# Optimization experiments

Measured on AMD Instinct MI355X. Metric: run time of the kernel, lower is better.

Reference implementation:

```python
import jax, jax.numpy as jnp
import numpy as np
from jax import lax

VOCAB, D, H, S, W, OUT = 100000, 300, 50, 64, 32, 5


def setup_inputs() -> dict:
    key = jax.random.key(0)
    ks = jax.random.split(key, 32)
    g = lambda i, shape, scale=0.05: (jax.random.normal(ks[i], shape, dtype=jnp.float32) * scale)
    inp = {
        'doc': jax.random.randint(ks[0], (S, W), 0, VOCAB),
        'emb': g(1, (VOCAB, D)),
        'wl_w': g(2, (H, D)), 'wl_b': g(3, (H,)),
        'c1_w': g(4, (H, H, 1)), 'c1_b': g(5, (H,)),
        'c2_w': g(6, (H, H, 2)), 'c2_b': g(7, (H,)),
        'c3_w': g(8, (H, H, 3)), 'c3_b': g(9, (H,)),
        'f_i_w': g(10, (H, 2 * H)), 'f_i_b': g(11, (H,)),
        'f_f_w': g(12, (H, 2 * H)), 'f_f_b': g(13, (H,)),
        'f_g_w': g(14, (H, 2 * H)), 'f_g_b': g(15, (H,)),
        'b_i_w': g(16, (H, 2 * H)), 'b_i_b': g(17, (H,)),
        'b_f_w': g(18, (H, 2 * H)), 'b_f_b': g(19, (H,)),
        'b_g_w': g(20, (H, 2 * H)), 'b_g_b': g(21, (H,)),
        'out_w': g(22, (OUT, 2 * H)), 'out_b': g(23, (OUT,)),
    }
    return inp


def _conv_rep(x, w, b):
    # x: [S, H, W]; w: [O, I, k] torch-style conv1d weight
    y = lax.conv_general_dilated(x, w, window_strides=(1,), padding='VALID',
                                 dimension_numbers=('NCH', 'OIH', 'NCH'))
    y = y + b[None, :, None]
    return jnp.tanh(y.mean(axis=2))  # [S, H]  (avg-pool over full length then tanh)


def _gnn_scan(reps, Wi, bi, Wf, bf, Wg, bg):
    # reps: [S, H]; sequential gated cell
    def step(h, r):
        comp = jnp.concatenate([r, h])  # [2H]
        i = jax.nn.sigmoid(comp @ Wi.T + bi)
        f = jax.nn.sigmoid(comp @ Wf.T + bf)
        g = jnp.tanh(comp @ Wg.T + bg)
        h_t = jnp.tanh(i * g + f * h)
        return h_t, h_t
    _, hs = lax.scan(step, jnp.zeros(reps.shape[1], dtype=reps.dtype), reps)
    return hs  # [S, H]


def reference(doc, emb, wl_w, wl_b, c1_w, c1_b, c2_w, c2_b, c3_w, c3_b,
              f_i_w, f_i_b, f_f_w, f_f_b, f_g_w, f_g_b,
              b_i_w, b_i_b, b_f_w, b_f_b, b_g_w, b_g_b, out_w, out_b):
    x = emb[doc]                                  # [S, W, D]
    p = jnp.einsum('swd,hd->swh', x, wl_w) + wl_b # word_linear, [S, W, H]
    xc = p.transpose(0, 2, 1)                     # [S, H, W]
    # sentence_convolution: mean over the 3 kernel-size branches
    rep = (_conv_rep(xc, c1_w, c1_b) + _conv_rep(xc, c2_w, c2_b) + _conv_rep(xc, c3_w, c3_b)) / 3.0
    h_f = _gnn_scan(rep, f_i_w, f_i_b, f_f_w, f_f_b, f_g_w, f_g_b)         # forward pass
    h_b = _gnn_scan(rep[::-1], b_i_w, b_i_b, b_f_w, b_f_b, b_g_w, b_g_b)[::-1]  # backward pass, realigned
    gnn_out = jnp.concatenate([h_f, h_b], axis=1).mean(axis=0)             # [2H]
    logits = gnn_out @ out_w.T + out_b
    return jax.nn.softmax(logits)
```

## Files before the change

### kernel.cpp

```cpp
#include <hip/hip_runtime.h>


__device__ __forceinline__ float rl(float v, int j) {
    return __uint_as_float((unsigned)__builtin_amdgcn_readlane(__float_as_uint(v), j));
}
__device__ __forceinline__ float sigm(float x) { return 1.f / (1.f + __expf(-x)); }
__device__ __forceinline__ float tanh_fast(float x) {
    return 1.f - 2.f / (__expf(2.f * x) + 1.f);
}

__global__ __launch_bounds__(320, 1) void rep_kernel(
    const int* __restrict__ doc, const float* __restrict__ emb,
    const float* __restrict__ wl_w, const float* __restrict__ wl_b,
    const float* __restrict__ c1w, const float* __restrict__ c1b,
    const float* __restrict__ c2w, const float* __restrict__ c2b,
    const float* __restrict__ c3w, const float* __restrict__ c3b,
    const float* __restrict__ fiw, const float* __restrict__ fib,
    const float* __restrict__ ffw, const float* __restrict__ ffb,
    const float* __restrict__ fgw, const float* __restrict__ fgb,
    const float* __restrict__ biw, const float* __restrict__ bib,
    const float* __restrict__ bfw, const float* __restrict__ bfb,
    const float* __restrict__ bgw, const float* __restrict__ bgb,
    float* __restrict__ preW)
{
    __shared__ int docs[32];
    __shared__ float xL[32][300];
    __shared__ float sv[5][300];
    __shared__ float P[5][50];
    __shared__ float m[6][50];
    __shared__ float r[50];

    const int s = blockIdx.x, tid = threadIdx.x;
    if (tid < 32) docs[tid] = doc[s * 32 + tid];
    __syncthreads();

    {
        const int w = tid / 10, part = tid - w * 10;
        const float2* row = (const float2*)(emb + docs[w] * 300);
#pragma unroll
        for (int t = 0; t < 15; ++t) {
            float2 v = row[part * 15 + t];
            const int d = (part * 15 + t) * 2;
            xL[w][d]     = v.x;
            xL[w][d + 1] = v.y;
        }
    }
    __syncthreads();

    if (tid < 300) {
        float a = 0.f;
#pragma unroll
        for (int w = 0; w < 32; ++w) a += xL[w][tid];
        sv[0][tid] = a;
        sv[1][tid] = xL[0][tid];
        sv[2][tid] = xL[1][tid];
        sv[3][tid] = xL[30][tid];
        sv[4][tid] = xL[31][tid];
    }
    __syncthreads();

    if (tid < 250) {
        const int i = tid / 5, v = tid - (tid / 5) * 5;
        const float2* wrow = (const float2*)(wl_w + i * 300);
        float a0 = 0.f, a1 = 0.f;
#pragma unroll 5
        for (int d2 = 0; d2 < 150; ++d2) {
            float2 wv = wrow[d2];
            a0 = fmaf(wv.x, sv[v][2 * d2],     a0);
            a1 = fmaf(wv.y, sv[v][2 * d2 + 1], a1);
        }
        P[v][i] = a0 + a1;
    }
    __syncthreads();

    if (tid < 50) {
        const int i = tid;
        const float b  = wl_b[i];
        const float QA = P[0][i], Q0 = P[1][i], Q1 = P[2][i],
                    Q30 = P[3][i], Q31 = P[4][i];
        m[0][i] = QA * (1.f / 32.f) + b;
        m[1][i] = (QA - Q31) * (1.f / 31.f) + b;
        m[2][i] = (QA - Q0)  * (1.f / 31.f) + b;
        m[3][i] = (QA - Q30 - Q31) * (1.f / 30.f) + b;
        m[4][i] = (QA - Q0  - Q31) * (1.f / 30.f) + b;
        m[5][i] = (QA - Q0  - Q1 ) * (1.f / 30.f) + b;
    }
    __syncthreads();

    if (tid < 50) {
        const int o = tid;
        float y1 = c1b[o], y2 = c2b[o], y3 = c3b[o];
        for (int i = 0; i < 50; ++i) {
            y1 = fmaf(c1w[o * 50 + i], m[0][i], y1);
            const float2 w2 = ((const float2*)c2w)[o * 50 + i];
            y2 = fmaf(w2.x, m[1][i], fmaf(w2.y, m[2][i], y2));
            y3 = fmaf(c3w[(o * 50 + i) * 3 + 0], m[3][i], y3);
            y3 = fmaf(c3w[(o * 50 + i) * 3 + 1], m[4][i], y3);
            y3 = fmaf(c3w[(o * 50 + i) * 3 + 2], m[5][i], y3);
        }
        r[o] = (tanh_fast(y1) + tanh_fast(y2) + tanh_fast(y3)) * (1.f / 3.f);
    }
    __syncthreads();

    if (tid < 300) {
        const int g = tid / 50, o = tid - g * 50;
        const float* Wg = (g == 0) ? fiw : (g == 1) ? ffw : (g == 2) ? fgw
                        : (g == 3) ? biw : (g == 4) ? bfw : bgw;
        const float* Bg = (g == 0) ? fib : (g == 1) ? ffb : (g == 2) ? fgb
                        : (g == 3) ? bib : (g == 4) ? bfb : bgb;
        const int sp = (g < 3) ? s : (63 - s);
        const float2* wrow = (const float2*)(Wg + o * 100);
        float acc = Bg[o];
#pragma unroll
        for (int j2 = 0; j2 < 25; ++j2) {
            float2 wv = wrow[j2];
            acc = fmaf(wv.x, r[2 * j2], fmaf(wv.y, r[2 * j2 + 1], acc));
        }
        preW[g * 3200 + sp * 50 + o] = acc;
    }
}

__global__ __launch_bounds__(384, 1) void scan_kernel(
    const float* __restrict__ preW,
    const float* __restrict__ fiw, const float* __restrict__ ffw,
    const float* __restrict__ fgw, const float* __restrict__ biw,
    const float* __restrict__ bfw, const float* __restrict__ bgw,
    const float* __restrict__ out_w, const float* __restrict__ out_b,
    float* __restrict__ outp)
{
    __shared__ float pre[6][64][50];
    __shared__ float aL[2][6][52];
    __shared__ float mh[2][52];
    __shared__ float lg[5];

    const int tid = threadIdx.x;
    const int wv = tid >> 6, lane = tid & 63;
    const int oc = (lane < 50) ? lane : 0;
    const int d  = (wv >= 3) ? 1 : 0;

    {
        const float2* src = (const float2*)preW;
        float2* dst = (float2*)&pre[0][0][0];
#pragma unroll
        for (int k = 0; k < 25; ++k) dst[tid + 384 * k] = src[tid + 384 * k];
    }

    const float* Wg = (wv == 0) ? fiw : (wv == 1) ? ffw : (wv == 2) ? fgw
                    : (wv == 3) ? biw : (wv == 4) ? bfw : bgw;
    float w[50];
    {
        const float2* wrow = (const float2*)(Wg + oc * 100 + 50);
#pragma unroll
        for (int j2 = 0; j2 < 25; ++j2) {
            float2 t = wrow[j2];
            w[2 * j2] = t.x; w[2 * j2 + 1] = t.y;
        }
    }
    __syncthreads();

    float h = 0.f, hsum = 0.f;
    float na = pre[wv][0][oc];
#pragma unroll 1
    for (int s2 = 0; s2 < 64; ++s2) {
        float a0 = na, a1 = 0.f, a2 = 0.f, a3 = 0.f;
        if (s2 < 63) na = pre[wv][s2 + 1][oc];
#pragma unroll
        for (int j = 0; j < 48; j += 4) {
            a0 = fmaf(w[j    ], rl(h, j    ), a0);
            a1 = fmaf(w[j + 1], rl(h, j + 1), a1);
            a2 = fmaf(w[j + 2], rl(h, j + 2), a2);
            a3 = fmaf(w[j + 3], rl(h, j + 3), a3);
        }
        a0 = fmaf(w[48], rl(h, 48), a0);
        a1 = fmaf(w[49], rl(h, 49), a1);
        const float a = (a0 + a1) + (a2 + a3);

        if (lane < 50) aL[s2 & 1][wv][lane] = a;
        __syncthreads();
        const float ai = aL[s2 & 1][d * 3 + 0][oc];
        const float af = aL[s2 & 1][d * 3 + 1][oc];
        const float ag = aL[s2 & 1][d * 3 + 2][oc];
        h = tanh_fast(fmaf(sigm(ai), tanh_fast(ag), sigm(af) * h));
        hsum += h;
    }
    if ((wv == 0 || wv == 3) && lane < 50) mh[d][lane] = hsum * (1.f / 64.f);
    __syncthreads();

    if (tid < 5) {
        const float2* wrow = (const float2*)(out_w + tid * 100);
        float acc = out_b[tid];
#pragma unroll
        for (int j2 = 0; j2 < 25; ++j2) {
            float2 wv2 = wrow[j2];
            acc = fmaf(wv2.x, mh[0][2 * j2], fmaf(wv2.y, mh[0][2 * j2 + 1], acc));
        }
#pragma unroll
        for (int j2 = 0; j2 < 25; ++j2) {
            float2 wv2 = wrow[25 + j2];
            acc = fmaf(wv2.x, mh[1][2 * j2], fmaf(wv2.y, mh[1][2 * j2 + 1], acc));
        }
        lg[tid] = acc;
    }
    __syncthreads();
    if (tid == 0) {
        float mx = lg[0];
#pragma unroll
        for (int k = 1; k < 5; ++k) mx = fmaxf(mx, lg[k]);
        float e[5], se = 0.f;
#pragma unroll
        for (int k = 0; k < 5; ++k) { e[k] = __expf(lg[k] - mx); se += e[k]; }
        const float inv = 1.f / se;
#pragma unroll
        for (int k = 0; k < 5; ++k) outp[k] = e[k] * inv;
    }
}

extern "C" void kernel_launch(void* const* d_in, const int* in_sizes, int n_in,
                              void* d_out, int out_size, void* d_ws, size_t ws_size,
                              hipStream_t stream)
{
    (void)in_sizes; (void)n_in; (void)out_size; (void)ws_size;
    const int*   doc  = (const int*)  d_in[0];
    const float* emb  = (const float*)d_in[1];
    const float* wl_w = (const float*)d_in[2];
    const float* wl_b = (const float*)d_in[3];
    const float* c1w  = (const float*)d_in[4];
    const float* c1b  = (const float*)d_in[5];
    const float* c2w  = (const float*)d_in[6];
    const float* c2b  = (const float*)d_in[7];
    const float* c3w  = (const float*)d_in[8];
    const float* c3b  = (const float*)d_in[9];
    const float* fiw  = (const float*)d_in[10];
    const float* fib  = (const float*)d_in[11];
    const float* ffw  = (const float*)d_in[12];
    const float* ffb  = (const float*)d_in[13];
    const float* fgw  = (const float*)d_in[14];
    const float* fgb  = (const float*)d_in[15];
    const float* biw  = (const float*)d_in[16];
    const float* bib  = (const float*)d_in[17];
    const float* bfw  = (const float*)d_in[18];
    const float* bfb  = (const float*)d_in[19];
    const float* bgw  = (const float*)d_in[20];
    const float* bgb  = (const float*)d_in[21];
    const float* ow   = (const float*)d_in[22];
    const float* ob   = (const float*)d_in[23];

    float* preW = (float*)d_ws;

    rep_kernel<<<64, 320, 0, stream>>>(doc, emb, wl_w, wl_b,
                                       c1w, c1b, c2w, c2b, c3w, c3b,
                                       fiw, fib, ffw, ffb, fgw, fgb,
                                       biw, bib, bfw, bfb, bgw, bgb, preW);
    scan_kernel<<<1, 384, 0, stream>>>(preW, fiw, ffw, fgw, biw, bfw, bgw,
                                       ow, ob, (float*)d_out);
}
```

Baseline: 266.8 us.

## Fuse scan gates per wave to drop per-step barrier, pack weights as fp16

The scan kernel now uses one wave per direction that computes all three gates itself. This removes the per-step LDS exchange and __syncthreads across six waves. To fit 150 recurrent weights in registers they are stored as packed half2, which adds rounding error to the recurrence. The rep kernel also gathers embeddings with float4 loads and splits the conv reductions across 300 threads with a partial-sum stage.

```diff
diff --git a/kernel.cpp b/kernel.cpp
--- a/kernel.cpp
+++ b/kernel.cpp
@@ -1,4 +1,5 @@
 #include <hip/hip_runtime.h>
+#include <hip/hip_fp16.h>
 
 
 __device__ __forceinline__ float rl(float v, int j) {
@@ -28,6 +29,7 @@
     __shared__ float sv[5][300];
     __shared__ float P[5][50];
     __shared__ float m[6][50];
+    __shared__ float part[6][50];
     __shared__ float r[50];
 
     const int s = blockIdx.x, tid = threadIdx.x;
@@ -35,14 +37,11 @@
     __syncthreads();
 
     {
-        const int w = tid / 10, part = tid - w * 10;
-        const float2* row = (const float2*)(emb + docs[w] * 300);
-#pragma unroll
-        for (int t = 0; t < 15; ++t) {
-            float2 v = row[part * 15 + t];
-            const int d = (part * 15 + t) * 2;
-            xL[w][d]     = v.x;
-            xL[w][d + 1] = v.y;
+        const float4* ef4 = (const float4*)emb;
+        float4* xf4 = (float4*)&xL[0][0];
+        for (int idx = tid; idx < 2400; idx += 320) {
+            const int rr = idx / 75, c = idx - rr * 75;
+            xf4[idx] = ef4[docs[rr] * 75 + c];
         }
     }
     __syncthreads();
@@ -87,18 +86,24 @@
     }
     __syncthreads();
 
+    if (tid < 300) {
+        const int q = tid / 50, o = tid - q * 50;
+        const float* base = (q == 0) ? c1w : (q < 3) ? c2w : c3w;
+        const int str = (q == 0) ? 1 : (q < 3) ? 2 : 3;
+        const int off = (q == 0) ? 0 : (q < 3) ? (q - 1) : (q - 3);
+        float acc = (q == 0) ? c1b[o] : (q == 1) ? c2b[o] : (q == 3) ? c3b[o] : 0.f;
+        const float* mp = m[q];
+#pragma unroll 5
+        for (int i = 0; i < 50; ++i)
+            acc = fmaf(base[(o * 50 + i) * str + off], mp[i], acc);
+        part[q][o] = acc;
+    }
+    __syncthreads();
     if (tid < 50) {
-        const int o = tid;
-        float y1 = c1b[o], y2 = c2b[o], y3 = c3b[o];
-        for (int i = 0; i < 50; ++i) {
-            y1 = fmaf(c1w[o * 50 + i], m[0][i], y1);
-            const float2 w2 = ((const float2*)c2w)[o * 50 + i];
-            y2 = fmaf(w2.x, m[1][i], fmaf(w2.y, m[2][i], y2));
-            y3 = fmaf(c3w[(o * 50 + i) * 3 + 0], m[3][i], y3);
-            y3 = fmaf(c3w[(o * 50 + i) * 3 + 1], m[4][i], y3);
-            y3 = fmaf(c3w[(o * 50 + i) * 3 + 2], m[5][i], y3);
-        }
-        r[o] = (tanh_fast(y1) + tanh_fast(y2) + tanh_fast(y3)) * (1.f / 3.f);
+        const float y1 = tanh_fast(part[0][tid]);
+        const float y2 = tanh_fast(part[1][tid] + part[2][tid]);
+        const float y3 = tanh_fast(part[3][tid] + part[4][tid] + part[5][tid]);
+        r[tid] = (y1 + y2 + y3) * (1.f / 3.f);
     }
     __syncthreads();
 
@@ -120,7 +125,7 @@
     }
 }
 
-__global__ __launch_bounds__(384, 1) void scan_kernel(
+__global__ __launch_bounds__(128, 1) void scan_kernel(
     const float* __restrict__ preW,
     const float* __restrict__ fiw, const float* __restrict__ ffw,
     const float* __restrict__ fgw, const float* __restrict__ biw,
@@ -129,61 +134,63 @@
     float* __restrict__ outp)
 {
     __shared__ float pre[6][64][50];
-    __shared__ float aL[2][6][52];
     __shared__ float mh[2][52];
     __shared__ float lg[5];
 
     const int tid = threadIdx.x;
-    const int wv = tid >> 6, lane = tid & 63;
+    const int d = tid >> 6, lane = tid & 63;
     const int oc = (lane < 50) ? lane : 0;
-    const int d  = (wv >= 3) ? 1 : 0;
 
     {
         const float2* src = (const float2*)preW;
         float2* dst = (float2*)&pre[0][0][0];
 #pragma unroll
-        for (int k = 0; k < 25; ++k) dst[tid + 384 * k] = src[tid + 384 * k];
-    }
-
-    const float* Wg = (wv == 0) ? fiw : (wv == 1) ? ffw : (wv == 2) ? fgw
-                    : (wv == 3) ? biw : (wv == 4) ? bfw : bgw;
-    float w[50];
+        for (int k = 0; k < 75; ++k) dst[tid + 128 * k] = src[tid + 128 * k];
+    }
+
+    const float* Wi = d ? biw : fiw;
+    const float* Wf = d ? bfw : ffw;
+    const float* Wg = d ? bgw : fgw;
+    __half2 hwi[25], hwf[25], hwg[25];
     {
-        const float2* wrow = (const float2*)(Wg + oc * 100 + 50);
-#pragma unroll
-        for (int j2 = 0; j2 < 25; ++j2) {
-            float2 t = wrow[j2];
-            w[2 * j2] = t.x; w[2 * j2 + 1] = t.y;
-        }
-    }
-    __syncthreads();
-
+        const float2* ri = (const float2*)(Wi + oc * 100 + 50);
+        const float2* rf = (const float2*)(Wf + oc * 100 + 50);
+        const float2* rg = (const float2*)(Wg + oc * 100 + 50);
+#pragma unroll
+        for (int k = 0; k < 25; ++k) {
+            float2 a = ri[k], b = rf[k], c = rg[k];
+            hwi[k] = __floats2half2_rn(a.x, a.y);
+            hwf[k] = __floats2half2_rn(b.x, b.y);
+            hwg[k] = __floats2half2_rn(c.x, c.y);
+        }
+    }
+    __syncthreads();
+
+    const int g0 = d * 3;
     float h = 0.f, hsum = 0.f;
-    float na = pre[wv][0][oc];
+    float nai = pre[g0 + 0][0][oc];
+    float naf = pre[g0 + 1][0][oc];
+    float nag = pre[g0 + 2][0][oc];
 #pragma unroll 1
     for (int s2 = 0; s2 < 64; ++s2) {
-        float a0 = na, a1 = 0.f, a2 = 0.f, a3 = 0.f;
-        if (s2 < 63) na = pre[wv][s2 + 1][oc];
-#pragma unroll
-        for (int j = 0; j < 48; j += 4) {
-            a0 = fmaf(w[j    ], rl(h, j    ), a0);
-            a1 = fmaf(w[j + 1], rl(h, j + 1), a1);
-            a2 = fmaf(w[j + 2], rl(h, j + 2), a2);
-            a3 = fmaf(w[j + 3], rl(h, j + 3), a3);
-        }
-        a0 = fmaf(w[48], rl(h, 48), a0);
-        a1 = fmaf(w[49], rl(h, 49), a1);
-        const float a = (a0 + a1) + (a2 + a3);
-
-        if (lane < 50) aL[s2 & 1][wv][lane] = a;
-        __syncthreads();
-        const float ai = aL[s2 & 1][d * 3 + 0][oc];
-        const float af = aL[s2 & 1][d * 3 + 1][oc];
-        const float ag = aL[s2 & 1][d * 3 + 2][oc];
+        float ai = nai, af = naf, ag = nag;
+        if (s2 < 63) {
+            nai = pre[g0 + 0][s2 + 1][oc];
+            naf = pre[g0 + 1][s2 + 1][oc];
+            nag = pre[g0 + 2][s2 + 1][oc];
+        }
+#pragma unroll
+        for (int k = 0; k < 25; ++k) {
+            const float h0 = rl(h, 2 * k);
+            const float h1 = rl(h, 2 * k + 1);
+            ai = fmaf(__low2float(hwi[k]), h0, fmaf(__high2float(hwi[k]), h1, ai));
+            af = fmaf(__low2float(hwf[k]), h0, fmaf(__high2float(hwf[k]), h1, af));
+            ag = fmaf(__low2float(hwg[k]), h0, fmaf(__high2float(hwg[k]), h1, ag));
+        }
         h = tanh_fast(fmaf(sigm(ai), tanh_fast(ag), sigm(af) * h));
         hsum += h;
     }
-    if ((wv == 0 || wv == 3) && lane < 50) mh[d][lane] = hsum * (1.f / 64.f);
+    if (lane < 50) mh[d][lane] = hsum * (1.f / 64.f);
     __syncthreads();
 
     if (tid < 5) {
@@ -251,6 +258,6 @@
                                        c1w, c1b, c2w, c2b, c3w, c3b,
                                        fiw, fib, ffw, ffb, fgw, fgb,
                                        biw, bib, bfw, bfb, bgw, bgb, preW);
-    scan_kernel<<<1, 384, 0, stream>>>(preW, fiw, ffw, fgw, biw, bfw, bgw,
+    scan_kernel<<<1, 128, 0, stream>>>(preW, fiw, ffw, fgw, biw, bfw, bgw,
                                        ow, ob, (float*)d_out);
 }
```

Result: faster. 258.8 us (-3.0%).
